# Kernel optimization log

Hardware: AMD Instinct MI355X
Metric: run time of the kernel (lower is better)

Reference implementation:

```python
import jax, jax.numpy as jnp
import numpy as np

N, E, D, H = 50000, 600000, 128, 256
EPS_DENOM = 1e-7   # epsilon added to sigmoid-edge denominator in the torch code
EPS_NORM = 1e-5    # InstanceNorm1d default eps


def _fcnn(x, Wa, ba, Wb, bb):
    # FCNN: Linear -> ReLU -> Linear
    return jax.nn.relu(x @ Wa + ba) @ Wb + bb


def setup_inputs() -> dict:
    key = jax.random.key(0)
    ks = jax.random.split(key, 16)
    inp = {
        "node_features": jax.random.normal(ks[0], (1, N, D), jnp.float32),
        "edge_index": jax.random.randint(ks[1], (1, 2, E), 0, N, dtype=jnp.int64)
        if jax.config.jax_enable_x64 else jax.random.randint(ks[1], (1, 2, E), 0, N, dtype=jnp.int32),
        "edge_features": jax.random.normal(ks[2], (1, E, D), jnp.float32),
        "global_features": jax.random.normal(ks[3], (1, 1, D), jnp.float32),
    }
    # three FCNNs: fc1 (D->H), fc2 (H->D), Kaiming-uniform-ish init scale 1/sqrt(fan_in)
    names = ["W1a", "b1a", "W1b", "b1b", "W2a", "b2a", "W2b", "b2b", "W3a", "b3a", "W3b", "b3b"]
    shapes = [(D, H), (H,), (H, D), (D,)] * 3
    fans = [D, D, H, H] * 3
    for k, (nm, sh, fan) in zip(ks[4:], zip(names, shapes, fans)):
        bound = 1.0 / np.sqrt(fan)
        inp[nm] = jax.random.uniform(k, sh, jnp.float32, -bound, bound)
    return inp


def reference(node_features, edge_index, edge_features, global_features,
              W1a, b1a, W1b, b1b, W2a, b2a, W2b, b2b, W3a, b3a, W3b, b3b):
    x = node_features[0]                      # [N, D]
    src = edge_index[0, 0]                    # [E]
    dst = edge_index[0, 1]                    # [E]
    s = jax.nn.sigmoid(edge_features[0])      # [E, D]

    # denominator: eps + sum of sigmoid(edge_feat) over all edges incident to node i
    denom = (EPS_DENOM
             + jax.ops.segment_sum(s, src, num_segments=N)
             + jax.ops.segment_sum(s, dst, num_segments=N))   # [N, D]

    h1 = _fcnn(x, W1a, b1a, W1b, b1b)                          # [N, D] self term
    h2 = _fcnn(x, W2a, b2a, W2b, b2b)                          # [N, D] neighbor term
    g3 = _fcnn(global_features[0, 0], W3a, b3a, W3b, b3b)      # [D]    global term

    # sum over incident edges of sigmoid(e) * FCNN_two(x_neighbor), then / denom
    agg = (jax.ops.segment_sum(s * h2[dst], src, num_segments=N)
           + jax.ops.segment_sum(s * h2[src], dst, num_segments=N))  # [N, D]

    inter = h1 + agg / denom + g3                              # [N, D]

    # InstanceNorm1d on a (1, D) vector: normalize over the feature dim (no affine)
    mu = jnp.mean(inter, axis=-1, keepdims=True)
    var = jnp.var(inter, axis=-1, keepdims=True)
    normed = (inter - mu) / jnp.sqrt(var + EPS_NORM)
    # dropout(p=0.1) treated as identity (inference mode)

    out = x + jax.nn.relu(normed)                              # residual update
    return out[None]                                           # [1, N, D]
```

## Files before the change

### kernel.cpp

```cpp
#include <hip/hip_runtime.h>
#include <math.h>

#define DD 128
#define HH 256

typedef __attribute__((ext_vector_type(8))) short bf16x8;
typedef __attribute__((ext_vector_type(4))) float f32x4;
typedef __attribute__((ext_vector_type(2))) float f32x2;
typedef unsigned short u16;
typedef unsigned int u32;
typedef unsigned char u8;

__device__ __forceinline__ float bf2f(u16 u) {
  union { u32 i; float f; } v; v.i = ((u32)u) << 16; return v.f;
}
__device__ __forceinline__ u16 f2bf(float f) {
  union { u32 i; float f; } v; v.f = f;
  u32 r = v.i + 0x7FFFu + ((v.i >> 16) & 1u);
  return (u16)(r >> 16);
}

#define GA_T 512
#define GA_C 512
__global__ __launch_bounds__(256) void mergeA(
    const float* __restrict__ W1a, const float* __restrict__ W1b,
    const float* __restrict__ W2a, const float* __restrict__ W2b,
    u16* __restrict__ o1, u16* __restrict__ o2,
    u16* __restrict__ o3, u16* __restrict__ o4,
    const float* __restrict__ gf,
    const float* __restrict__ W3a, const float* __restrict__ b3a,
    const float* __restrict__ W3b, const float* __restrict__ b3b,
    float* __restrict__ g3out,
    const int* __restrict__ eix, u32* __restrict__ deg,
    u32* __restrict__ posrec, int twoE) {
  const int b = blockIdx.x;
  if (b < GA_T) {
    int idx = b * 256 + threadIdx.x;
    int m = idx >> 15;
    int r = idx & 32767;
    const float* in; u16* out; int K, Nc;
    if (m == 0)      { in = W1a; out = o1; K = DD; Nc = HH; }
    else if (m == 1) { in = W1b; out = o2; K = HH; Nc = DD; }
    else if (m == 2) { in = W2a; out = o3; K = DD; Nc = HH; }
    else             { in = W2b; out = o4; K = HH; Nc = DD; }
    int k = r / Nc, n = r % Nc;
    out[n * K + k] = f2bf(in[r]);
  } else if (b == GA_T) {
    __shared__ float gs[DD];
    __shared__ float hs[HH];
    int t = threadIdx.x;
    if (t < DD) gs[t] = gf[t];
    __syncthreads();
    float acc = b3a[t];
    for (int k = 0; k < DD; ++k) acc = fmaf(gs[k], W3a[k * HH + t], acc);
    hs[t] = acc > 0.f ? acc : 0.f;
    __syncthreads();
    if (t < DD) {
      float o = b3b[t];
      for (int j = 0; j < HH; ++j) o = fmaf(hs[j], W3b[j * DD + t], o);
      g3out[t] = o;
    }
  } else {
    int t = (b - GA_T - 1) * 256 + threadIdx.x;
    const int stride = GA_C * 256;
    for (; t < twoE; t += stride) posrec[t] = atomicAdd(&deg[eix[t]], 1u);
  }
}

__global__ __launch_bounds__(1024) void scan_kernel(const u32* __restrict__ deg,
    u32* __restrict__ rowstart, int N) {
  __shared__ u32 wsum[16];
  const int t = threadIdx.x;
  const int w = t >> 6, lane = t & 63;
  const int span = ((N + 1023) & ~1023) >> 4;
  const int b = w * span;
  const int e = min(b + span, N);

  u32 s = 0;
  for (int i = b + lane; i < e; i += 64) s += deg[i];
#pragma unroll
  for (int off = 32; off; off >>= 1) s += __shfl_xor(s, off);
  if (lane == 0) wsum[w] = s;
  __syncthreads();

  u32 carry = 0;
  for (int i = 0; i < w; ++i) carry += wsum[i];

  for (int i0 = b; i0 < e; i0 += 64) {
    int i = i0 + lane;
    u32 v = (i < e) ? deg[i] : 0u;
    u32 inc = v;
#pragma unroll
    for (int off = 1; off < 64; off <<= 1) {
      u32 u2 = __shfl_up(inc, off);
      if (lane >= off) inc += u2;
    }
    u32 excl = carry + inc - v;
    if (i < e) rowstart[i] = excl;
    carry += __shfl(inc, 63);
  }
  if (w == 15 && lane == 63) rowstart[N] = carry;
}

__global__ __launch_bounds__(256) void gemm_l1(const float* __restrict__ x,
    const u16* __restrict__ w1aT, const float* __restrict__ b1a,
    const u16* __restrict__ w2aT, const float* __restrict__ b2a,
    u16* __restrict__ hid, int M) {
  const int wave = (blockIdx.x * 256 + threadIdx.x) >> 6;
  const int lane = threadIdx.x & 63;
  const int totalWaves = (gridDim.x * 256) >> 6;
  const int nc = wave & 7;
  const int mw = wave >> 3;
  const int mStride = totalWaves >> 3;
  const int which = nc >> 2;
  const int c0 = (nc & 3) * 64;
  const u16* wT = which ? w2aT : w1aT;
  const float* bs = which ? b2a : b1a;
  const int l15 = lane & 15, l4 = lane >> 4;

  bf16x8 bfrag[4][4];
  float bcol[4];
#pragma unroll
  for (int t = 0; t < 4; ++t) {
    const int col = c0 + t * 16 + l15;
    const u16* bb = wT + (size_t)col * DD + l4 * 8;
#pragma unroll
    for (int kb = 0; kb < 4; ++kb) bfrag[kb][t] = *(const bf16x8*)(bb + kb * 32);
    bcol[t] = bs[col];
  }

  const int mTiles = (M + 15) >> 4;
  for (int mt = mw; mt < mTiles; mt += mStride) {
    const int m0 = mt << 4;
    int rowA = m0 + l15; if (rowA >= M) rowA = M - 1;
    const float* xr = x + (size_t)rowA * DD + l4 * 8;
    bf16x8 ax[4];
#pragma unroll
    for (int kb = 0; kb < 4; ++kb) {
      f32x4 a = *(const f32x4*)(xr + kb * 32);
      f32x4 b = *(const f32x4*)(xr + kb * 32 + 4);
      bf16x8 v;
      v[0] = (short)f2bf(a.x); v[1] = (short)f2bf(a.y);
      v[2] = (short)f2bf(a.z); v[3] = (short)f2bf(a.w);
      v[4] = (short)f2bf(b.x); v[5] = (short)f2bf(b.y);
      v[6] = (short)f2bf(b.z); v[7] = (short)f2bf(b.w);
      ax[kb] = v;
    }
    f32x4 acc[4] = {{0,0,0,0},{0,0,0,0},{0,0,0,0},{0,0,0,0}};
#pragma unroll
    for (int kb = 0; kb < 4; ++kb)
#pragma unroll
      for (int t = 0; t < 4; ++t)
        acc[t] = __builtin_amdgcn_mfma_f32_16x16x32_bf16(ax[kb], bfrag[kb][t], acc[t], 0, 0, 0);
#pragma unroll
    for (int t = 0; t < 4; ++t)
#pragma unroll
      for (int r = 0; r < 4; ++r) {
        const int row = m0 + l4 * 4 + r;
        float v = acc[t][r] + bcol[t];
        v = v > 0.f ? v : 0.f;
        if (row < M) hid[(size_t)row * 512 + which * 256 + c0 + t * 16 + l15] = f2bf(v);
      }
  }
}

__global__ __launch_bounds__(256) void gemm_l2(const u16* __restrict__ hid,
    const u16* __restrict__ w1bT, const float* __restrict__ b1b,
    const u16* __restrict__ w2bT, const float* __restrict__ b2b,
    u16* __restrict__ h1, u8* __restrict__ h28, int M) {
  const int wave = (blockIdx.x * 256 + threadIdx.x) >> 6;
  const int lane = threadIdx.x & 63;
  const int totalWaves = (gridDim.x * 256) >> 6;
  const int nc = wave & 3;
  const int mw = wave >> 2;
  const int mStride = totalWaves >> 2;
  const int which = nc >> 1;
  const int c0 = (nc & 1) * 64;
  const u16* wT = which ? w2bT : w1bT;
  const float* bs = which ? b2b : b1b;
  const int l15 = lane & 15, l4 = lane >> 4;

  bf16x8 bfrag[8][4];
  float bcol[4];
#pragma unroll
  for (int t = 0; t < 4; ++t) {
    const int col = c0 + t * 16 + l15;
    const u16* bb = wT + (size_t)col * HH + l4 * 8;
#pragma unroll
    for (int kb = 0; kb < 8; ++kb) bfrag[kb][t] = *(const bf16x8*)(bb + kb * 32);
    bcol[t] = bs[col];
  }

  const int mTiles = (M + 15) >> 4;
  for (int mt = mw; mt < mTiles; mt += mStride) {
    const int m0 = mt << 4;
    int rowA = m0 + l15; if (rowA >= M) rowA = M - 1;
    const u16* arow = hid + (size_t)rowA * 512 + which * 256 + l4 * 8;
    f32x4 acc[4] = {{0,0,0,0},{0,0,0,0},{0,0,0,0},{0,0,0,0}};
#pragma unroll
    for (int kb = 0; kb < 8; ++kb) {
      bf16x8 afrag = *(const bf16x8*)(arow + kb * 32);
#pragma unroll
      for (int t = 0; t < 4; ++t)
        acc[t] = __builtin_amdgcn_mfma_f32_16x16x32_bf16(afrag, bfrag[kb][t], acc[t], 0, 0, 0);
    }
#pragma unroll
    for (int t = 0; t < 4; ++t)
#pragma unroll
      for (int r = 0; r < 4; ++r) {
        const int row = m0 + l4 * 4 + r;
        if (row >= M) continue;
        float v = acc[t][r] + bcol[t];
        const int col = c0 + t * 16 + l15;
        if (which) {
          u32 w = (u32)__builtin_amdgcn_cvt_pk_fp8_f32(v, v, 0, false);
          h28[(size_t)row * DD + col] = (u8)(w & 0xffu);
        } else {
          h1[(size_t)row * DD + col] = f2bf(v);
        }
      }
  }
}

#define SS_SIG  4096
#define SS_SCAT 1024
__global__ __launch_bounds__(256) void mergeSS3(
    const float* __restrict__ ef, uint2* __restrict__ s8, int n8,
    const int* __restrict__ eix, const u32* __restrict__ rowstart,
    const u32* __restrict__ posrec, uint2* __restrict__ adj, int E) {
  const int b = blockIdx.x;
  if (b < SS_SIG) {
    int i = b * 256 + threadIdx.x;
    const int stride = SS_SIG * 256;
    for (; i < n8; i += stride) {
      const f32x4 a = __builtin_nontemporal_load(((const f32x4*)ef) + i * 2);
      const f32x4 bb = __builtin_nontemporal_load(((const f32x4*)ef) + i * 2 + 1);
      float s0 = 1.f / (1.f + __expf(-a.x));
      float s1 = 1.f / (1.f + __expf(-a.y));
      float s2 = 1.f / (1.f + __expf(-a.z));
      float s3 = 1.f / (1.f + __expf(-a.w));
      float s4 = 1.f / (1.f + __expf(-bb.x));
      float s5 = 1.f / (1.f + __expf(-bb.y));
      float s6 = 1.f / (1.f + __expf(-bb.z));
      float s7 = 1.f / (1.f + __expf(-bb.w));
      u32 w0 = (u32)__builtin_amdgcn_cvt_pk_fp8_f32(s0, s1, 0, false);
      w0 = (u32)__builtin_amdgcn_cvt_pk_fp8_f32(s2, s3, (int)w0, true);
      u32 w1 = (u32)__builtin_amdgcn_cvt_pk_fp8_f32(s4, s5, 0, false);
      w1 = (u32)__builtin_amdgcn_cvt_pk_fp8_f32(s6, s7, (int)w1, true);
      s8[i] = make_uint2(w0, w1);
    }
  } else {
    int t = (b - SS_SIG) * 256 + threadIdx.x;
    const int stride = SS_SCAT * 256;
    const int twoE = 2 * E;
    for (; t < twoE; t += stride) {
      int node, eid, other;
      if (t < E) { node = eix[t]; eid = t;     other = eix[t + E]; }
      else       { node = eix[t]; eid = t - E; other = eix[t - E]; }
      u32 pos = rowstart[node] + posrec[t];
      adj[pos] = make_uint2((u32)eid, (u32)other);
    }
  }
}

__global__ __launch_bounds__(256) void gather_fp8(const float* __restrict__ x,
    const u16* __restrict__ h1, const u8* __restrict__ h28,
    const u8* __restrict__ s8, const uint2* __restrict__ adj,
    const u32* __restrict__ rowstart, const float* __restrict__ g3,
    float* __restrict__ out, int N) {
  int row0 = (blockIdx.x * 256 + threadIdx.x) >> 6;
  if (row0 >= N) return;
  const int row = __builtin_amdgcn_readfirstlane(row0);
  const int lane = threadIdx.x & 63;
  const int d0 = lane * 2;

  const u32 beg = rowstart[row];
  const u32 end = rowstart[row + 1];

  float dx = 0.f, dy = 0.f, ax = 0.f, ay = 0.f;
  u32 j = beg;
  for (; j + 8 <= end; j += 8) {
    uint2 e[8];
    u32 sv[8], hv[8];
#pragma unroll
    for (int q = 0; q < 8; ++q) e[q] = adj[j + q];
#pragma unroll
    for (int q = 0; q < 8; ++q) {
      sv[q] = *(const u16*)(s8  + (size_t)e[q].x * DD + d0);
      hv[q] = *(const u16*)(h28 + (size_t)e[q].y * DD + d0);
    }
#pragma unroll
    for (int q = 0; q < 8; ++q) {
      f32x2 sf = __builtin_amdgcn_cvt_pk_f32_fp8((int)sv[q], false);
      f32x2 hf = __builtin_amdgcn_cvt_pk_f32_fp8((int)hv[q], false);
      dx += sf.x; dy += sf.y;
      ax = fmaf(sf.x, hf.x, ax);
      ay = fmaf(sf.y, hf.y, ay);
    }
  }
  for (; j < end; ++j) {
    uint2 en = adj[j];
    u32 sv = *(const u16*)(s8  + (size_t)en.x * DD + d0);
    u32 hv = *(const u16*)(h28 + (size_t)en.y * DD + d0);
    f32x2 sf = __builtin_amdgcn_cvt_pk_f32_fp8((int)sv, false);
    f32x2 hf = __builtin_amdgcn_cvt_pk_f32_fp8((int)hv, false);
    dx += sf.x; dy += sf.y;
    ax = fmaf(sf.x, hf.x, ax);
    ay = fmaf(sf.y, hf.y, ay);
  }

  const size_t base = (size_t)row * DD + d0;
  f32x2 xv = __builtin_nontemporal_load((const f32x2*)(x + base));
  u32 h1u = __builtin_nontemporal_load((const u32*)(h1 + base));
  f32x2 gv = *(const f32x2*)(g3 + d0);

  float i0 = bf2f((u16)(h1u & 0xffffu)) + ax / (dx + 1e-7f) + gv.x;
  float i1 = bf2f((u16)(h1u >> 16)) + ay / (dy + 1e-7f) + gv.y;

  float s = i0 + i1;
  float q = i0 * i0 + i1 * i1;
#pragma unroll
  for (int off = 32; off; off >>= 1) {
    s += __shfl_xor(s, off);
    q += __shfl_xor(q, off);
  }
  float mean = s * (1.f / 128.f);
  float var = q * (1.f / 128.f) - mean * mean;
  float rstd = rsqrtf(var + 1e-5f);
  float n0v = (i0 - mean) * rstd;
  float n1v = (i1 - mean) * rstd;
  f32x2 ov;
  ov.x = xv.x + (n0v > 0.f ? n0v : 0.f);
  ov.y = xv.y + (n1v > 0.f ? n1v : 0.f);
  __builtin_nontemporal_store(ov, (f32x2*)(out + base));
}

extern "C" void kernel_launch(void* const* d_in, const int* in_sizes, int n_in,
                              void* d_out, int out_size, void* d_ws, size_t ws_size,
                              hipStream_t stream) {
  const float* x   = (const float*)d_in[0];
  const int*   eix = (const int*)d_in[1];
  const float* ef  = (const float*)d_in[2];
  const float* gf  = (const float*)d_in[3];
  const float* W1a = (const float*)d_in[4];
  const float* b1a = (const float*)d_in[5];
  const float* W1b = (const float*)d_in[6];
  const float* b1b = (const float*)d_in[7];
  const float* W2a = (const float*)d_in[8];
  const float* b2a = (const float*)d_in[9];
  const float* W2b = (const float*)d_in[10];
  const float* b2b = (const float*)d_in[11];
  const float* W3a = (const float*)d_in[12];
  const float* b3a = (const float*)d_in[13];
  const float* W3b = (const float*)d_in[14];
  const float* b3b = (const float*)d_in[15];

  const int N = in_sizes[0] / DD;
  const int E = in_sizes[2] / DD;

  char* p = (char*)d_ws;
  auto take = [&](size_t bytes) -> char* {
    char* r = p;
    p += (bytes + 255) & ~(size_t)255;
    return r;
  };
  u16* w1aT   = (u16*)take((size_t)DD * HH * 2);
  u16* w1bT   = (u16*)take((size_t)DD * HH * 2);
  u16* w2aT   = (u16*)take((size_t)DD * HH * 2);
  u16* w2bT   = (u16*)take((size_t)DD * HH * 2);
  u16* hidb   = (u16*)take((size_t)N * 512 * 2);
  u16* h1b    = (u16*)take((size_t)N * DD * 2);
  u32* deg    = (u32*)take((size_t)N * 4);
  u32* rowst  = (u32*)take((size_t)(N + 1) * 4);
  u32* posrec = (u32*)take((size_t)2 * E * 4);
  float* g3   = (float*)take((size_t)DD * 4);
  uint2* adj  = (uint2*)take((size_t)2 * E * 8);
  u8* s8      = (u8*)take((size_t)E * DD);
  u8* h28     = (u8*)take((size_t)N * DD);

  hipMemsetAsync(deg, 0, (size_t)N * 4, stream);

  mergeA<<<GA_T + 1 + GA_C, 256, 0, stream>>>(W1a, W1b, W2a, W2b,
                                              w1aT, w1bT, w2aT, w2bT,
                                              gf, W3a, b3a, W3b, b3b, g3,
                                              eix, deg, posrec, 2 * E);
  scan_kernel<<<1, 1024, 0, stream>>>(deg, rowst, N);

  gemm_l1<<<2048, 256, 0, stream>>>(x, w1aT, b1a, w2aT, b2a, hidb, N);
  gemm_l2<<<2048, 256, 0, stream>>>(hidb, w1bT, b1b, w2bT, b2b, h1b, h28, N);

  mergeSS3<<<SS_SIG + SS_SCAT, 256, 0, stream>>>(ef, (uint2*)s8, E * DD / 8,
                                                 eix, rowst, posrec, adj, E);

  gather_fp8<<<(N + 3) / 4, 256, 0, stream>>>(x, h1b, h28, s8, adj, rowst, g3,
                                              (float*)d_out, N);
}
```

Before: 345.6 us.

## Move adjacency scatter into layer-1 GEMM launch and deepen gather unrolling

The CSR adjacency scatter leaves the sigmoid/fp8 kernel and runs as extra blocks inside the first GEMM launch, so its memory-bound scattered writes can overlap with GEMM compute. Sigmoid now runs in its own kernel. The gather loop now handles 16 edges per step, then 4, then 1, and reads adjacency entries as 64-bit nontemporal loads, putting more independent loads in flight. Extra scatter blocks may compete with GEMM blocks for compute units, and the larger unroll raises register pressure.

```diff
diff --git a/kernel.cpp b/kernel.cpp
--- a/kernel.cpp
+++ b/kernel.cpp
@@ -9,6 +9,7 @@
 typedef __attribute__((ext_vector_type(2))) float f32x2;
 typedef unsigned short u16;
 typedef unsigned int u32;
+typedef unsigned long long u64;
 typedef unsigned char u8;
 
 __device__ __forceinline__ float bf2f(u16 u) {
@@ -102,13 +103,29 @@
   if (w == 15 && lane == 63) rowstart[N] = carry;
 }
 
-__global__ __launch_bounds__(256) void gemm_l1(const float* __restrict__ x,
+#define L1_GEMM 2048
+#define L1_SCAT 512
+__global__ __launch_bounds__(256) void gemm_l1_scat(const float* __restrict__ x,
     const u16* __restrict__ w1aT, const float* __restrict__ b1a,
     const u16* __restrict__ w2aT, const float* __restrict__ b2a,
-    u16* __restrict__ hid, int M) {
+    u16* __restrict__ hid, int M,
+    const int* __restrict__ eix, const u32* __restrict__ rowstart,
+    const u32* __restrict__ posrec, uint2* __restrict__ adj, int E) {
+  if (blockIdx.x >= L1_GEMM) {
+    int t = (blockIdx.x - L1_GEMM) * 256 + threadIdx.x;
+    const int stride = L1_SCAT * 256;
+    const int twoE = 2 * E;
+    for (; t < twoE; t += stride) {
+      int node, eid, other;
+      if (t < E) { node = eix[t]; eid = t;     other = eix[t + E]; }
+      else       { node = eix[t]; eid = t - E; other = eix[t - E]; }
+      adj[rowstart[node] + posrec[t]] = make_uint2((u32)eid, (u32)other);
+    }
+    return;
+  }
   const int wave = (blockIdx.x * 256 + threadIdx.x) >> 6;
   const int lane = threadIdx.x & 63;
-  const int totalWaves = (gridDim.x * 256) >> 6;
+  const int totalWaves = L1_GEMM * 4;
   const int nc = wave & 7;
   const int mw = wave >> 3;
   const int mStride = totalWaves >> 3;
@@ -222,50 +239,41 @@
   }
 }
 
-#define SS_SIG  4096
-#define SS_SCAT 1024
-__global__ __launch_bounds__(256) void mergeSS3(
-    const float* __restrict__ ef, uint2* __restrict__ s8, int n8,
-    const int* __restrict__ eix, const u32* __restrict__ rowstart,
-    const u32* __restrict__ posrec, uint2* __restrict__ adj, int E) {
-  const int b = blockIdx.x;
-  if (b < SS_SIG) {
-    int i = b * 256 + threadIdx.x;
-    const int stride = SS_SIG * 256;
-    for (; i < n8; i += stride) {
-      const f32x4 a = __builtin_nontemporal_load(((const f32x4*)ef) + i * 2);
-      const f32x4 bb = __builtin_nontemporal_load(((const f32x4*)ef) + i * 2 + 1);
-      float s0 = 1.f / (1.f + __expf(-a.x));
-      float s1 = 1.f / (1.f + __expf(-a.y));
-      float s2 = 1.f / (1.f + __expf(-a.z));
-      float s3 = 1.f / (1.f + __expf(-a.w));
-      float s4 = 1.f / (1.f + __expf(-bb.x));
-      float s5 = 1.f / (1.f + __expf(-bb.y));
-      float s6 = 1.f / (1.f + __expf(-bb.z));
-      float s7 = 1.f / (1.f + __expf(-bb.w));
-      u32 w0 = (u32)__builtin_amdgcn_cvt_pk_fp8_f32(s0, s1, 0, false);
-      w0 = (u32)__builtin_amdgcn_cvt_pk_fp8_f32(s2, s3, (int)w0, true);
-      u32 w1 = (u32)__builtin_amdgcn_cvt_pk_fp8_f32(s4, s5, 0, false);
-      w1 = (u32)__builtin_amdgcn_cvt_pk_fp8_f32(s6, s7, (int)w1, true);
-      s8[i] = make_uint2(w0, w1);
-    }
-  } else {
-    int t = (b - SS_SIG) * 256 + threadIdx.x;
-    const int stride = SS_SCAT * 256;
-    const int twoE = 2 * E;
-    for (; t < twoE; t += stride) {
-      int node, eid, other;
-      if (t < E) { node = eix[t]; eid = t;     other = eix[t + E]; }
-      else       { node = eix[t]; eid = t - E; other = eix[t - E]; }
-      u32 pos = rowstart[node] + posrec[t];
-      adj[pos] = make_uint2((u32)eid, (u32)other);
-    }
-  }
+__global__ __launch_bounds__(256) void sigmoid_fp8(const float* __restrict__ ef,
+                                                   uint2* __restrict__ s8, int n8) {
+  int i = blockIdx.x * 256 + threadIdx.x;
+  const int stride = gridDim.x * 256;
+  for (; i < n8; i += stride) {
+    const f32x4 a = __builtin_nontemporal_load(((const f32x4*)ef) + i * 2);
+    const f32x4 bb = __builtin_nontemporal_load(((const f32x4*)ef) + i * 2 + 1);
+    float s0 = 1.f / (1.f + __expf(-a.x));
+    float s1 = 1.f / (1.f + __expf(-a.y));
+    float s2 = 1.f / (1.f + __expf(-a.z));
+    float s3 = 1.f / (1.f + __expf(-a.w));
+    float s4 = 1.f / (1.f + __expf(-bb.x));
+    float s5 = 1.f / (1.f + __expf(-bb.y));
+    float s6 = 1.f / (1.f + __expf(-bb.z));
+    float s7 = 1.f / (1.f + __expf(-bb.w));
+    u32 w0 = (u32)__builtin_amdgcn_cvt_pk_fp8_f32(s0, s1, 0, false);
+    w0 = (u32)__builtin_amdgcn_cvt_pk_fp8_f32(s2, s3, (int)w0, true);
+    u32 w1 = (u32)__builtin_amdgcn_cvt_pk_fp8_f32(s4, s5, 0, false);
+    w1 = (u32)__builtin_amdgcn_cvt_pk_fp8_f32(s6, s7, (int)w1, true);
+    s8[i] = make_uint2(w0, w1);
+  }
+}
+
+__device__ __forceinline__ void acc_fp8(u32 sv, u32 hv, float& dx, float& dy,
+                                        float& ax, float& ay) {
+  f32x2 sf = __builtin_amdgcn_cvt_pk_f32_fp8((int)sv, false);
+  f32x2 hf = __builtin_amdgcn_cvt_pk_f32_fp8((int)hv, false);
+  dx += sf.x; dy += sf.y;
+  ax = fmaf(sf.x, hf.x, ax);
+  ay = fmaf(sf.y, hf.y, ay);
 }
 
 __global__ __launch_bounds__(256) void gather_fp8(const float* __restrict__ x,
     const u16* __restrict__ h1, const u8* __restrict__ h28,
-    const u8* __restrict__ s8, const uint2* __restrict__ adj,
+    const u8* __restrict__ s8, const u64* __restrict__ adj,
     const u32* __restrict__ rowstart, const float* __restrict__ g3,
     float* __restrict__ out, int N) {
   int row0 = (blockIdx.x * 256 + threadIdx.x) >> 6;
@@ -279,34 +287,37 @@
 
   float dx = 0.f, dy = 0.f, ax = 0.f, ay = 0.f;
   u32 j = beg;
-  for (; j + 8 <= end; j += 8) {
-    uint2 e[8];
-    u32 sv[8], hv[8];
-#pragma unroll
-    for (int q = 0; q < 8; ++q) e[q] = adj[j + q];
-#pragma unroll
-    for (int q = 0; q < 8; ++q) {
-      sv[q] = *(const u16*)(s8  + (size_t)e[q].x * DD + d0);
-      hv[q] = *(const u16*)(h28 + (size_t)e[q].y * DD + d0);
-    }
-#pragma unroll
-    for (int q = 0; q < 8; ++q) {
-      f32x2 sf = __builtin_amdgcn_cvt_pk_f32_fp8((int)sv[q], false);
-      f32x2 hf = __builtin_amdgcn_cvt_pk_f32_fp8((int)hv[q], false);
-      dx += sf.x; dy += sf.y;
-      ax = fmaf(sf.x, hf.x, ax);
-      ay = fmaf(sf.y, hf.y, ay);
-    }
+  for (; j + 16 <= end; j += 16) {
+    u64 e[16];
+    u32 sv[16], hv[16];
+#pragma unroll
+    for (int q = 0; q < 16; ++q) e[q] = __builtin_nontemporal_load(adj + j + q);
+#pragma unroll
+    for (int q = 0; q < 16; ++q) {
+      sv[q] = *(const u16*)(s8  + (size_t)(u32)e[q] * DD + d0);
+      hv[q] = *(const u16*)(h28 + (size_t)(u32)(e[q] >> 32) * DD + d0);
+    }
+#pragma unroll
+    for (int q = 0; q < 16; ++q) acc_fp8(sv[q], hv[q], dx, dy, ax, ay);
+  }
+  for (; j + 4 <= end; j += 4) {
+    u64 e[4];
+    u32 sv[4], hv[4];
+#pragma unroll
+    for (int q = 0; q < 4; ++q) e[q] = __builtin_nontemporal_load(adj + j + q);
+#pragma unroll
+    for (int q = 0; q < 4; ++q) {
+      sv[q] = *(const u16*)(s8  + (size_t)(u32)e[q] * DD + d0);
+      hv[q] = *(const u16*)(h28 + (size_t)(u32)(e[q] >> 32) * DD + d0);
+    }
+#pragma unroll
+    for (int q = 0; q < 4; ++q) acc_fp8(sv[q], hv[q], dx, dy, ax, ay);
   }
   for (; j < end; ++j) {
-    uint2 en = adj[j];
-    u32 sv = *(const u16*)(s8  + (size_t)en.x * DD + d0);
-    u32 hv = *(const u16*)(h28 + (size_t)en.y * DD + d0);
-    f32x2 sf = __builtin_amdgcn_cvt_pk_f32_fp8((int)sv, false);
-    f32x2 hf = __builtin_amdgcn_cvt_pk_f32_fp8((int)hv, false);
-    dx += sf.x; dy += sf.y;
-    ax = fmaf(sf.x, hf.x, ax);
-    ay = fmaf(sf.y, hf.y, ay);
+    u64 e = __builtin_nontemporal_load(adj + j);
+    u32 sv = *(const u16*)(s8  + (size_t)(u32)e * DD + d0);
+    u32 hv = *(const u16*)(h28 + (size_t)(u32)(e >> 32) * DD + d0);
+    acc_fp8(sv, hv, dx, dy, ax, ay);
   }
 
   const size_t base = (size_t)row * DD + d0;
@@ -386,12 +397,13 @@
                                               eix, deg, posrec, 2 * E);
   scan_kernel<<<1, 1024, 0, stream>>>(deg, rowst, N);
 
-  gemm_l1<<<2048, 256, 0, stream>>>(x, w1aT, b1a, w2aT, b2a, hidb, N);
+  gemm_l1_scat<<<L1_GEMM + L1_SCAT, 256, 0, stream>>>(x, w1aT, b1a, w2aT, b2a,
+                                                      hidb, N,
+                                                      eix, rowst, posrec, adj, E);
   gemm_l2<<<2048, 256, 0, stream>>>(hidb, w1bT, b1b, w2bT, b2b, h1b, h28, N);
 
-  mergeSS3<<<SS_SIG + SS_SCAT, 256, 0, stream>>>(ef, (uint2*)s8, E * DD / 8,
-                                                 eix, rowst, posrec, adj, E);
-
-  gather_fp8<<<(N + 3) / 4, 256, 0, stream>>>(x, h1b, h28, s8, adj, rowst, g3,
-                                              (float*)d_out, N);
-}
+  sigmoid_fp8<<<4096, 256, 0, stream>>>(ef, (uint2*)s8, E * DD / 8);
+
+  gather_fp8<<<(N + 3) / 4, 256, 0, stream>>>(x, h1b, h28, s8, (const u64*)adj,
+                                              rowst, g3, (float*)d_out, N);
+}
```

Result: no change. 339.5 us (median of 2 runs) (-1.7%).
